# Kernel tuning notes

Measured on AMD Instinct MI355X. Metric: run time of the kernel, lower is better.

## Reference

```python
import jax, jax.numpy as jnp
import numpy as np

NUM_HEADS = 16
NUM_T = 8
L1D = 16  # img_size // patch_size


def _freqs_1d(dim, end, base=10000.0):
    f = 1.0 / (base ** (jnp.arange(0, dim, 2, dtype=jnp.float32) / dim))  # [dim/2]
    ang = jnp.outer(jnp.arange(end, dtype=jnp.float32), f)                # [end, dim/2]
    return jnp.cos(ang), jnp.sin(ang)


def _freqs_2d(dim, h, w, base=10000.0):
    f = 1.0 / (base ** (jnp.arange(0, dim, 4, dtype=jnp.float32)[: dim // 4] / dim))  # [dim/4]
    ax = jnp.outer(jnp.arange(w, dtype=jnp.float32), f)  # [w, dim/4]
    ay = jnp.outer(jnp.arange(h, dtype=jnp.float32), f)  # [h, dim/4]
    # flatten order: position index = y*w + x
    ang_x = jnp.broadcast_to(ax[None, :, :], (h, w, dim // 4)).reshape(h * w, dim // 4)
    ang_y = jnp.broadcast_to(ay[:, None, :], (h, w, dim // 4)).reshape(h * w, dim // 4)
    ang = jnp.concatenate([ang_x, ang_y], axis=-1)  # [h*w, dim/2]
    return jnp.cos(ang), jnp.sin(ang)


def _rope(x, cos, sin):
    # x: [..., P, d]; cos/sin: [P, d/2]; interleaved complex pairs (x0,x1),(x2,x3),...
    xr, xi = x[..., 0::2], x[..., 1::2]
    or_ = xr * cos - xi * sin
    oi = xr * sin + xi * cos
    return jnp.stack([or_, oi], axis=-1).reshape(x.shape)


def setup_inputs() -> dict:
    key = jax.random.key(0)
    ks = jax.random.split(key, 5)
    H = 1024
    return {
        "x": jax.random.normal(ks[0], (2, 2048, H), dtype=jnp.float32),
        "w_qkv": jax.random.normal(ks[1], (3 * H, H), dtype=jnp.float32) * 0.02,
        "b_qkv": jax.random.normal(ks[2], (3 * H,), dtype=jnp.float32) * 0.02,
        "w_out": jax.random.normal(ks[3], (H, H), dtype=jnp.float32) * 0.02,
        "b_out": jax.random.normal(ks[4], (H,), dtype=jnp.float32) * 0.02,
    }


def reference(x, w_qkv, b_qkv, w_out, b_out):
    B, L, H = x.shape
    n, t = NUM_HEADS, NUM_T
    hd = H // n
    Ls = L // t  # spatial tokens per frame (= L1D*L1D)

    # QKV projection; per-head layout [q|k|v] of size 3*hd (matches torch rearrange+chunk)
    qkv = (x @ w_qkv.T + b_qkv).reshape(B, L, n, 3 * hd)
    q, k, v = qkv[..., :hd], qkv[..., hd:2 * hd], qkv[..., 2 * hd:]

    cos_s, sin_s = _freqs_2d(hd, L1D, L1D)  # [Ls, hd/2]
    cos_t, sin_t = _freqs_1d(hd, t)         # [t, hd/2]

    def to_bntl(a):  # (B, L=t*Ls, n, hd) -> (B, n, t, Ls, hd)
        return a.reshape(B, t, Ls, n, hd).transpose(0, 3, 1, 2, 4)

    q = _rope(to_bntl(q), cos_s, sin_s)
    k = _rope(to_bntl(k), cos_s, sin_s)
    # temporal rope: rotate over t axis
    q = _rope(q.transpose(0, 1, 3, 2, 4), cos_t, sin_t).transpose(0, 1, 3, 2, 4)
    k = _rope(k.transpose(0, 1, 3, 2, 4), cos_t, sin_t).transpose(0, 1, 3, 2, 4)
    q = q.reshape(B, n, L, hd)
    k = k.reshape(B, n, L, hd)
    v = v.transpose(0, 2, 1, 3)  # (B, n, L, hd)

    scores = jnp.einsum('bnqd,bnkd->bnqk', q, k) / jnp.sqrt(jnp.asarray(hd, jnp.float32))
    idx = jnp.arange(L)
    neg = jnp.finfo(jnp.float32).min
    causal = jnp.where(idx[None, :] <= idx[:, None], 0.0, neg)  # [L, L]
    attn = jax.nn.softmax((scores + causal).astype(jnp.float32), axis=-1).astype(x.dtype)

    o = jnp.einsum('bnqk,bnkd->bnqd', attn, v).transpose(0, 2, 1, 3).reshape(B, L, H)
    o = o * jax.nn.sigmoid(o)  # swish
    return o @ w_out.T + b_out
```

## Files before the change

kernel.cpp:

```cpp
#include <hip/hip_runtime.h>
#include <math.h>

#define B_SZ 2
#define L_SEQ 2048
#define H_SZ 1024
#define NH 16
#define HD 64
#define QSCALE 0.18033688011112042f

typedef __attribute__((ext_vector_type(8))) short frag_ab;
typedef __attribute__((ext_vector_type(4))) float frag_cd;
typedef __attribute__((ext_vector_type(8))) unsigned short u16x8;
typedef __attribute__((ext_vector_type(4))) unsigned short u16x4;

__device__ __forceinline__ unsigned short f2bf(float f) {
  unsigned int x = __builtin_bit_cast(unsigned int, f);
  x += 0x7fffu + ((x >> 16) & 1u);
  return (unsigned short)(x >> 16);
}
__device__ __forceinline__ float bf2f(unsigned int u) {
  return __builtin_bit_cast(float, u << 16);
}
__device__ __forceinline__ unsigned int cvt_pk_bf16(float lo, float hi) {
  unsigned int r;
  asm("v_cvt_pk_bf16_f32 %0, %1, %2" : "=v"(r) : "v"(lo), "v"(hi));
  return r;
}
__device__ __forceinline__ void gload16(const void* g, void* l) {
  __builtin_amdgcn_global_load_lds((const __attribute__((address_space(1))) void*)g,
                                   (__attribute__((address_space(3))) void*)l, 16, 0, 0);
}

__device__ __forceinline__ void cvt8(const float* __restrict__ in,
                                     unsigned short* __restrict__ out, int i) {
  float4 a = *(const float4*)&in[i];
  float4 b = *(const float4*)&in[i + 4];
  u16x8 o = {f2bf(a.x), f2bf(a.y), f2bf(a.z), f2bf(a.w),
             f2bf(b.x), f2bf(b.y), f2bf(b.z), f2bf(b.w)};
  *(u16x8*)&out[i] = o;
}

__global__ __launch_bounds__(256) void glue_pre_k(
    const float* __restrict__ x, const float* __restrict__ wq, const float* __restrict__ wo,
    unsigned short* __restrict__ xb, unsigned short* __restrict__ wqb,
    unsigned short* __restrict__ wob, float2* __restrict__ ctab) {
  int bx = blockIdx.x, tid = threadIdx.x;
  if (bx < 256) {
    int idx = bx * 256 + tid;
    int l = idx >> 5, j = idx & 31;
    int ti = l >> 8;
    int s = l & 255;
    float ang_s;
    if (j < 16) ang_s = (float)(s & 15) * powf(10000.f, -(float)j / 16.f);
    else        ang_s = (float)(s >> 4) * powf(10000.f, -(float)(j - 16) / 16.f);
    float ang_t = (float)ti * powf(10000.f, -(float)j / 32.f);
    float a = ang_s + ang_t;
    ctab[idx] = make_float2(cosf(a), sinf(a));
  } else if (bx < 2304) {
    cvt8(x, xb, ((bx - 256) * 256 + tid) * 8);
  } else if (bx < 3840) {
    cvt8(wq, wqb, ((bx - 2304) * 256 + tid) * 8);
  } else {
    cvt8(wo, wob, ((bx - 3840) * 256 + tid) * 8);
  }
}

#define G_ISSUE(k0, bi)                                                        \
  _Pragma("unroll") for (int it = 0; it < 2; ++it) {                           \
    int c = tid + it * 256;                                                    \
    int row = c >> 2, e0 = (c & 3) * 8;                                        \
    gload16(A + (size_t)(m0 + row) * K + (k0) + e0, &As[bi][c * 8]);           \
    gload16(W + (size_t)(n0 + row) * K + (k0) + e0, &Ws[bi][c * 8]);           \
  }

__global__ __launch_bounds__(256) void gemm_qkv_fused_k(
    const unsigned short* __restrict__ A, const unsigned short* __restrict__ W,
    const float* __restrict__ bias, const float2* __restrict__ ctab,
    unsigned short* __restrict__ Qb, unsigned short* __restrict__ Kb,
    unsigned short* __restrict__ Vt) {
  const int K = 1024, N = 3072;
  __shared__ unsigned short As[2][128 * 32];
  __shared__ unsigned short Ws[2][128 * 32];
  const frag_cd fzero = {0.f, 0.f, 0.f, 0.f};
  int tid = threadIdx.x;
  int nbx = N >> 7;
  int nwg = gridDim.x;
  int bid = blockIdx.x;
  int qq = nwg >> 3;
  int bidx = (bid & 7) * qq + (bid >> 3);
  int m0 = (bidx / nbx) * 128, n0 = (bidx % nbx) * 128;
  int w = tid >> 6, lane = tid & 63, t = lane & 15, g = lane >> 4;
  int wm = w >> 1, wn = w & 1;
  frag_cd acc[4][4];
#pragma unroll
  for (int mi = 0; mi < 4; ++mi)
#pragma unroll
    for (int ni = 0; ni < 4; ++ni) acc[mi][ni] = fzero;

  G_ISSUE(0, 0);
  __syncthreads();
  int kb = 0;
  for (int k0 = 0; k0 < K; k0 += 32, kb ^= 1) {
    if (k0 + 32 < K) { G_ISSUE(k0 + 32, kb ^ 1); }
    frag_ab af[4], wf[4];
#pragma unroll
    for (int mi = 0; mi < 4; ++mi)
      af[mi] = *(const frag_ab*)&As[kb][(wm * 64 + mi * 16 + t) * 32 + 8 * g];
#pragma unroll
    for (int ni = 0; ni < 4; ++ni)
      wf[ni] = *(const frag_ab*)&Ws[kb][(wn * 64 + ni * 16 + t) * 32 + 8 * g];
    __builtin_amdgcn_s_setprio(1);
#pragma unroll
    for (int mi = 0; mi < 4; ++mi)
#pragma unroll
      for (int ni = 0; ni < 4; ++ni)
        acc[mi][ni] = __builtin_amdgcn_mfma_f32_16x16x32_bf16(af[mi], wf[ni], acc[mi][ni], 0, 0, 0);
    __builtin_amdgcn_s_setprio(0);
    __syncthreads();
  }

#pragma unroll
  for (int ni = 0; ni < 4; ++ni) {
    int cb = n0 + wn * 64 + ni * 16;
    int region = (cb >> 6) % 3;
    int head = cb / 192;
    int d = (cb & 63) + t;
    float bv = bias[cb + t];
    if (region == 2) {
#pragma unroll
      for (int mi = 0; mi < 4; ++mi) {
        int row0 = m0 + wm * 64 + mi * 16 + g * 4;
        int bb = row0 >> 11, l0 = row0 & 2047;
        u16x4 ov;
#pragma unroll
        for (int r = 0; r < 4; ++r) ov[r] = f2bf(acc[mi][ni][r] + bv);
        *(u16x4*)&Vt[((size_t)((bb * NH + head) * HD + d)) * L_SEQ + l0] = ov;
      }
    } else {
      float qs = (region == 0) ? QSCALE : 1.f;
      float sgn = (t & 1) ? qs : -qs;
      unsigned short* dst = (region == 0) ? Qb : Kb;
      int j = d >> 1;
#pragma unroll
      for (int mi = 0; mi < 4; ++mi) {
        int row0 = m0 + wm * 64 + mi * 16 + g * 4;
        int bb = row0 >> 11, l0 = row0 & 2047;
        size_t obase = ((size_t)(bb * NH + head) * L_SEQ + l0) * HD + d;
#pragma unroll
        for (int r = 0; r < 4; ++r) {
          float v = acc[mi][ni][r] + bv;
          float p = __shfl_xor(v, 1);
          float2 cs = ctab[(l0 + r) * 32 + j];
          float o = v * (cs.x * qs) + p * (cs.y * sgn);
          dst[obase + (size_t)r * HD] = f2bf(o);
        }
      }
    }
  }
}

__global__ __launch_bounds__(256) void gemm_mfma_k(
    const unsigned short* __restrict__ A, const unsigned short* __restrict__ W,
    const float* __restrict__ bias, float* __restrict__ C, int M, int N, int K) {
  __shared__ unsigned short As[2][128 * 32];
  __shared__ unsigned short Ws[2][128 * 32];
  const frag_cd fzero = {0.f, 0.f, 0.f, 0.f};
  int tid = threadIdx.x;
  int nbx = N >> 7;
  int nwg = gridDim.x;
  int bid = blockIdx.x;
  int qq = nwg >> 3;
  int bidx = (bid & 7) * qq + (bid >> 3);
  int m0 = (bidx / nbx) * 128, n0 = (bidx % nbx) * 128;
  int w = tid >> 6, lane = tid & 63, t = lane & 15, g = lane >> 4;
  int wm = w >> 1, wn = w & 1;
  frag_cd acc[4][4];
#pragma unroll
  for (int mi = 0; mi < 4; ++mi)
#pragma unroll
    for (int ni = 0; ni < 4; ++ni) acc[mi][ni] = fzero;

  G_ISSUE(0, 0);
  __syncthreads();
  int kb = 0;
  for (int k0 = 0; k0 < K; k0 += 32, kb ^= 1) {
    if (k0 + 32 < K) { G_ISSUE(k0 + 32, kb ^ 1); }
    frag_ab af[4], wf[4];
#pragma unroll
    for (int mi = 0; mi < 4; ++mi)
      af[mi] = *(const frag_ab*)&As[kb][(wm * 64 + mi * 16 + t) * 32 + 8 * g];
#pragma unroll
    for (int ni = 0; ni < 4; ++ni)
      wf[ni] = *(const frag_ab*)&Ws[kb][(wn * 64 + ni * 16 + t) * 32 + 8 * g];
    __builtin_amdgcn_s_setprio(1);
#pragma unroll
    for (int mi = 0; mi < 4; ++mi)
#pragma unroll
      for (int ni = 0; ni < 4; ++ni)
        acc[mi][ni] = __builtin_amdgcn_mfma_f32_16x16x32_bf16(af[mi], wf[ni], acc[mi][ni], 0, 0, 0);
    __builtin_amdgcn_s_setprio(0);
    __syncthreads();
  }
#pragma unroll
  for (int mi = 0; mi < 4; ++mi)
#pragma unroll
    for (int ni = 0; ni < 4; ++ni) {
      int col = n0 + wn * 64 + ni * 16 + t;
      float bv = bias[col];
#pragma unroll
      for (int r = 0; r < 4; ++r)
        C[(size_t)(m0 + wm * 64 + mi * 16 + g * 4 + r) * N + col] = acc[mi][ni][r] + bv;
    }
}

__device__ __forceinline__ void attn_tile(
    const unsigned short* __restrict__ Ksb, const unsigned short* __restrict__ Vsb,
    unsigned short* __restrict__ pw,
    const frag_ab* qf, frag_cd* oacc, float& l_run,
    int qrow, bool diag, int kt, int t, int g) {
  const frag_cd cinit = {-32.f, -32.f, -32.f, -32.f};
  frag_cd st[4];
  __builtin_amdgcn_s_setprio(1);
#pragma unroll
  for (int kb = 0; kb < 4; ++kb) {
    frag_ab k0f = *(const frag_ab*)&Ksb[(((kb * 16 + t) * 64) + 8 * g) ^ ((t & 7) << 3)];
    frag_ab k1f = *(const frag_ab*)&Ksb[(((kb * 16 + t) * 64) + 32 + 8 * g) ^ ((t & 7) << 3)];
    st[kb] = __builtin_amdgcn_mfma_f32_16x16x32_bf16(k0f, qf[0], cinit, 0, 0, 0);
    st[kb] = __builtin_amdgcn_mfma_f32_16x16x32_bf16(k1f, qf[1], st[kb], 0, 0, 0);
  }
  __builtin_amdgcn_s_setprio(0);
  float sv[16];
#pragma unroll
  for (int kb = 0; kb < 4; ++kb)
#pragma unroll
    for (int r = 0; r < 4; ++r) {
      float x = st[kb][r];
      if (diag && (kt * 64 + kb * 16 + g * 4 + r) > qrow) x = -1e30f;
      sv[kb * 4 + r] = x;
    }
  float psum = 0.f;
  unsigned int pk[8];
#pragma unroll
  for (int i = 0; i < 8; ++i) {
    float p0 = __builtin_amdgcn_exp2f(sv[2 * i]);
    float p1 = __builtin_amdgcn_exp2f(sv[2 * i + 1]);
    psum += p0 + p1;
    pk[i] = cvt_pk_bf16(p0, p1);
  }
  psum += __shfl_xor(psum, 16);
  psum += __shfl_xor(psum, 32);
  l_run += psum;

#pragma unroll
  for (int kb = 0; kb < 4; ++kb) {
    uint2 pr = {pk[kb * 2], pk[kb * 2 + 1]};
    *(uint2*)&pw[(t * 64 + kb * 16 + g * 4) ^ ((t & 7) << 3)] = pr;
  }
  frag_ab pf0 = *(const frag_ab*)&pw[(t * 64 + 8 * g) ^ ((t & 7) << 3)];
  frag_ab pf1 = *(const frag_ab*)&pw[(t * 64 + 32 + 8 * g) ^ ((t & 7) << 3)];
  const frag_cd fzero = {0.f, 0.f, 0.f, 0.f};
  (void)fzero;
  __builtin_amdgcn_s_setprio(1);
#pragma unroll
  for (int db = 0; db < 4; ++db) {
    frag_ab v0f = *(const frag_ab*)&Vsb[(((db * 16 + t) * 64) + 8 * g) ^ ((t & 7) << 3)];
    frag_ab v1f = *(const frag_ab*)&Vsb[(((db * 16 + t) * 64) + 32 + 8 * g) ^ ((t & 7) << 3)];
    oacc[db] = __builtin_amdgcn_mfma_f32_16x16x32_bf16(v0f, pf0, oacc[db], 0, 0, 0);
    oacc[db] = __builtin_amdgcn_mfma_f32_16x16x32_bf16(v1f, pf1, oacc[db], 0, 0, 0);
  }
  __builtin_amdgcn_s_setprio(0);
}

__global__ __launch_bounds__(512) void attn_mfma_k(
    const unsigned short* __restrict__ Qg, const unsigned short* __restrict__ Kg,
    const unsigned short* __restrict__ Vt, unsigned short* __restrict__ Og) {
  __shared__ unsigned short Ks[2][64 * 64];
  __shared__ unsigned short Vs[2][64 * 64];
  __shared__ unsigned short Ps[8][16 * 64];
  const frag_cd fzero = {0.f, 0.f, 0.f, 0.f};
  int bx = blockIdx.x;
  int qtA = bx & 15;
  int n = (bx >> 4) & 15;
  int b = bx >> 8;
  int qtB = 31 - qtA;
  int tid = threadIdx.x;
  int w = tid >> 6, lane = tid & 63, t = lane & 15, g = lane >> 4;
  int side = w >> 2;
  int qt = side ? qtA : qtB;
  size_t kvbase = ((size_t)(b * NH + n)) * L_SEQ * HD;
  int qrow = qt * 64 + (w & 3) * 16 + t;

  const unsigned short* qp = Qg + kvbase + (size_t)qrow * HD;
  frag_ab qf[2] = {*(const frag_ab*)(qp + 8 * g), *(const frag_ab*)(qp + 32 + 8 * g)};

  frag_cd oacc[4];
#pragma unroll
  for (int db = 0; db < 4; ++db) oacc[db] = fzero;
  float l_run = 0.f;

  int srow = tid >> 3, se0 = (tid & 7) * 8;
  int sdst = (srow * 64 + se0) ^ ((srow & 7) << 3);
  u16x8 kreg = *(const u16x8*)(Kg + kvbase + (size_t)srow * HD + se0);
  u16x8 vreg = *(const u16x8*)(Vt + kvbase + (size_t)srow * L_SEQ + se0);
  *(u16x8*)&Ks[0][sdst] = kreg;
  *(u16x8*)&Vs[0][sdst] = vreg;

  for (int kt = 0; kt <= qtB; ++kt) {
    int cur = kt & 1;
    __syncthreads();
    if (kt < qtB) {
      kreg = *(const u16x8*)(Kg + kvbase + (size_t)((kt + 1) * 64 + srow) * HD + se0);
      vreg = *(const u16x8*)(Vt + kvbase + (size_t)srow * L_SEQ + (kt + 1) * 64 + se0);
    }
    if (kt <= qt)
      attn_tile(&Ks[cur][0], &Vs[cur][0], &Ps[w][0], qf, oacc, l_run, qrow,
                kt == qt, kt, t, g);
    if (kt < qtB) {
      int nxt = cur ^ 1;
      *(u16x8*)&Ks[nxt][sdst] = kreg;
      *(u16x8*)&Vs[nxt][sdst] = vreg;
    }
  }

  size_t ob0 = (size_t)b * L_SEQ * H_SZ + n * 64;
  float inv = 1.f / l_run;
#pragma unroll
  for (int db = 0; db < 4; ++db) {
    u16x4 ov;
#pragma unroll
    for (int r = 0; r < 4; ++r) {
      float o = oacc[db][r] * inv;
      o = o / (1.f + __expf(-o));
      ov[r] = f2bf(o);
    }
    *(u16x4*)&Og[ob0 + (size_t)qrow * H_SZ + db * 16 + g * 4] = ov;
  }
}

extern "C" void kernel_launch(void* const* d_in, const int* in_sizes, int n_in,
                              void* d_out, int out_size, void* d_ws, size_t ws_size,
                              hipStream_t stream) {
  const float* x = (const float*)d_in[0];
  const float* w_qkv = (const float*)d_in[1];
  const float* b_qkv = (const float*)d_in[2];
  const float* w_out = (const float*)d_in[3];
  const float* b_out = (const float*)d_in[4];
  float* out = (float*)d_out;

  float* ws = (float*)d_ws;
  float2* ctab = (float2*)ws;
  unsigned short* us = (unsigned short*)(ws + 131072);
  unsigned short* Qb = us;
  unsigned short* Kb = Qb + 4194304;
  unsigned short* Vt = Kb + 4194304;
  unsigned short* Og = Vt + 4194304;
  unsigned short* xb = Og + 4194304;
  unsigned short* wqkvb = xb + 4194304;
  unsigned short* woutb = wqkvb + 3145728;

  glue_pre_k<<<4352, 256, 0, stream>>>(x, w_qkv, w_out, xb, wqkvb, woutb, ctab);

  gemm_qkv_fused_k<<<768, 256, 0, stream>>>(xb, wqkvb, b_qkv, ctab, Qb, Kb, Vt);

  attn_mfma_k<<<B_SZ * NH * 16, 512, 0, stream>>>(Qb, Kb, Vt, Og);

  gemm_mfma_k<<<256, 256, 0, stream>>>(Og, woutb, b_out, out, 4096, 1024, 1024);
}
```

Baseline: 113.1 us.

## Software-pipeline attention QK^T one tile ahead with triple-buffered K/V

The attention loop now computes QK^T scores for the next key tile before doing softmax and PV on the current tile, using a three-slot K/V shared buffer and prefetching two tiles ahead. This is meant to overlap MFMA score work with the exp/pack and PV phase and to cut barrier stalls, at the cost of more registers and LDS. Separately, the RoPE cos/sin table is transposed to a j-major layout so the QKV epilogue reads four consecutive positions with two float4 loads instead of four strided float2 loads.

```diff
diff --git a/kernel.cpp b/kernel.cpp
--- a/kernel.cpp
+++ b/kernel.cpp
@@ -47,7 +47,7 @@
   int bx = blockIdx.x, tid = threadIdx.x;
   if (bx < 256) {
     int idx = bx * 256 + tid;
-    int l = idx >> 5, j = idx & 31;
+    int j = idx >> 11, l = idx & 2047;
     int ti = l >> 8;
     int s = l & 255;
     float ang_s;
@@ -146,12 +146,16 @@
         int row0 = m0 + wm * 64 + mi * 16 + g * 4;
         int bb = row0 >> 11, l0 = row0 & 2047;
         size_t obase = ((size_t)(bb * NH + head) * L_SEQ + l0) * HD + d;
+        const float2* cp = ctab + (size_t)j * 2048 + l0;
+        float4 v01 = *(const float4*)cp;
+        float4 v23 = *(const float4*)(cp + 2);
+        float cvec[4] = {v01.x, v01.z, v23.x, v23.z};
+        float svec[4] = {v01.y, v01.w, v23.y, v23.w};
 #pragma unroll
         for (int r = 0; r < 4; ++r) {
           float v = acc[mi][ni][r] + bv;
           float p = __shfl_xor(v, 1);
-          float2 cs = ctab[(l0 + r) * 32 + j];
-          float o = v * (cs.x * qs) + p * (cs.y * sgn);
+          float o = v * (cvec[r] * qs) + p * (svec[r] * sgn);
           dst[obase + (size_t)r * HD] = f2bf(o);
         }
       }
@@ -213,13 +217,10 @@
     }
 }
 
-__device__ __forceinline__ void attn_tile(
-    const unsigned short* __restrict__ Ksb, const unsigned short* __restrict__ Vsb,
-    unsigned short* __restrict__ pw,
-    const frag_ab* qf, frag_cd* oacc, float& l_run,
-    int qrow, bool diag, int kt, int t, int g) {
+__device__ __forceinline__ void qk_compute(
+    const unsigned short* __restrict__ Ksb, const frag_ab* qf, frag_cd* st,
+    int t, int g) {
   const frag_cd cinit = {-32.f, -32.f, -32.f, -32.f};
-  frag_cd st[4];
   __builtin_amdgcn_s_setprio(1);
 #pragma unroll
   for (int kb = 0; kb < 4; ++kb) {
@@ -229,21 +230,24 @@
     st[kb] = __builtin_amdgcn_mfma_f32_16x16x32_bf16(k1f, qf[1], st[kb], 0, 0, 0);
   }
   __builtin_amdgcn_s_setprio(0);
-  float sv[16];
-#pragma unroll
-  for (int kb = 0; kb < 4; ++kb)
-#pragma unroll
-    for (int r = 0; r < 4; ++r) {
-      float x = st[kb][r];
-      if (diag && (kt * 64 + kb * 16 + g * 4 + r) > qrow) x = -1e30f;
-      sv[kb * 4 + r] = x;
-    }
+}
+
+__device__ __forceinline__ void sm_pv(
+    const unsigned short* __restrict__ Vsb, unsigned short* __restrict__ pw,
+    const frag_cd* st, frag_cd* oacc, float& l_run,
+    int qrow, bool diag, int kt, int t, int g) {
   float psum = 0.f;
   unsigned int pk[8];
 #pragma unroll
   for (int i = 0; i < 8; ++i) {
-    float p0 = __builtin_amdgcn_exp2f(sv[2 * i]);
-    float p1 = __builtin_amdgcn_exp2f(sv[2 * i + 1]);
+    int kb = i >> 1, r0 = (2 * i) & 3;
+    float x0 = st[kb][r0], x1 = st[kb][r0 + 1];
+    if (diag) {
+      if ((kt * 64 + kb * 16 + g * 4 + r0) > qrow) x0 = -1e30f;
+      if ((kt * 64 + kb * 16 + g * 4 + r0 + 1) > qrow) x1 = -1e30f;
+    }
+    float p0 = __builtin_amdgcn_exp2f(x0);
+    float p1 = __builtin_amdgcn_exp2f(x1);
     psum += p0 + p1;
     pk[i] = cvt_pk_bf16(p0, p1);
   }
@@ -258,8 +262,6 @@
   }
   frag_ab pf0 = *(const frag_ab*)&pw[(t * 64 + 8 * g) ^ ((t & 7) << 3)];
   frag_ab pf1 = *(const frag_ab*)&pw[(t * 64 + 32 + 8 * g) ^ ((t & 7) << 3)];
-  const frag_cd fzero = {0.f, 0.f, 0.f, 0.f};
-  (void)fzero;
   __builtin_amdgcn_s_setprio(1);
 #pragma unroll
   for (int db = 0; db < 4; ++db) {
@@ -274,8 +276,8 @@
 __global__ __launch_bounds__(512) void attn_mfma_k(
     const unsigned short* __restrict__ Qg, const unsigned short* __restrict__ Kg,
     const unsigned short* __restrict__ Vt, unsigned short* __restrict__ Og) {
-  __shared__ unsigned short Ks[2][64 * 64];
-  __shared__ unsigned short Vs[2][64 * 64];
+  __shared__ unsigned short Ks[3][64 * 64];
+  __shared__ unsigned short Vs[3][64 * 64];
   __shared__ unsigned short Ps[8][16 * 64];
   const frag_cd fzero = {0.f, 0.f, 0.f, 0.f};
   int bx = blockIdx.x;
@@ -289,6 +291,7 @@
   int qt = side ? qtA : qtB;
   size_t kvbase = ((size_t)(b * NH + n)) * L_SEQ * HD;
   int qrow = qt * 64 + (w & 3) * 16 + t;
+  unsigned short* pw = &Ps[w][0];
 
   const unsigned short* qp = Qg + kvbase + (size_t)qrow * HD;
   frag_ab qf[2] = {*(const frag_ab*)(qp + 8 * g), *(const frag_ab*)(qp + 32 + 8 * g)};
@@ -300,26 +303,37 @@
 
   int srow = tid >> 3, se0 = (tid & 7) * 8;
   int sdst = (srow * 64 + se0) ^ ((srow & 7) << 3);
+
   u16x8 kreg = *(const u16x8*)(Kg + kvbase + (size_t)srow * HD + se0);
   u16x8 vreg = *(const u16x8*)(Vt + kvbase + (size_t)srow * L_SEQ + se0);
   *(u16x8*)&Ks[0][sdst] = kreg;
   *(u16x8*)&Vs[0][sdst] = vreg;
-
+  kreg = *(const u16x8*)(Kg + kvbase + (size_t)(64 + srow) * HD + se0);
+  vreg = *(const u16x8*)(Vt + kvbase + (size_t)srow * L_SEQ + 64 + se0);
+  __syncthreads();
+
+  frag_cd st[4], stN[4];
+  qk_compute(&Ks[0][0], qf, st, t, g);
+
+  int cur = 0;
   for (int kt = 0; kt <= qtB; ++kt) {
-    int cur = kt & 1;
-    __syncthreads();
+    int nxt = (cur == 2) ? 0 : cur + 1;
     if (kt < qtB) {
-      kreg = *(const u16x8*)(Kg + kvbase + (size_t)((kt + 1) * 64 + srow) * HD + se0);
-      vreg = *(const u16x8*)(Vt + kvbase + (size_t)srow * L_SEQ + (kt + 1) * 64 + se0);
-    }
-    if (kt <= qt)
-      attn_tile(&Ks[cur][0], &Vs[cur][0], &Ps[w][0], qf, oacc, l_run, qrow,
-                kt == qt, kt, t, g);
-    if (kt < qtB) {
-      int nxt = cur ^ 1;
       *(u16x8*)&Ks[nxt][sdst] = kreg;
       *(u16x8*)&Vs[nxt][sdst] = vreg;
     }
+    __syncthreads();
+    if (kt + 1 < qtB) {
+      kreg = *(const u16x8*)(Kg + kvbase + (size_t)((kt + 2) * 64 + srow) * HD + se0);
+      vreg = *(const u16x8*)(Vt + kvbase + (size_t)srow * L_SEQ + (kt + 2) * 64 + se0);
+    }
+    if (kt < qtB && kt + 1 <= qt)
+      qk_compute(&Ks[nxt][0], qf, stN, t, g);
+    if (kt <= qt)
+      sm_pv(&Vs[cur][0], pw, st, oacc, l_run, qrow, kt == qt, kt, t, g);
+#pragma unroll
+    for (int kb = 0; kb < 4; ++kb) st[kb] = stN[kb];
+    cur = nxt;
   }
 
   size_t ob0 = (size_t)b * L_SEQ * H_SZ + n * 64;
```

Result: no change. 115.2 us (+1.8%).

## Process four query tiles per attention block and transpose RoPE table layout

Applied to the files above, without the earlier changes.

The attention kernel now has each workgroup handle four query tiles (two long, two short, paired across the causal triangle) instead of two. Each wave keeps two sets of accumulators and two Q fragments, and every K/V tile loaded into shared memory is reused by both. The grid is halved, which roughly halves total K/V global traffic at the cost of higher register pressure and fewer workgroups. Separately, the cos/sin table is stored frequency-major so the QKV epilogue can load four consecutive rows with vector loads, and the masking loop is folded into the exp loop.

```diff
diff --git a/kernel.cpp b/kernel.cpp
--- a/kernel.cpp
+++ b/kernel.cpp
@@ -47,7 +47,7 @@
   int bx = blockIdx.x, tid = threadIdx.x;
   if (bx < 256) {
     int idx = bx * 256 + tid;
-    int l = idx >> 5, j = idx & 31;
+    int j = idx >> 11, l = idx & 2047;
     int ti = l >> 8;
     int s = l & 255;
     float ang_s;
@@ -146,12 +146,16 @@
         int row0 = m0 + wm * 64 + mi * 16 + g * 4;
         int bb = row0 >> 11, l0 = row0 & 2047;
         size_t obase = ((size_t)(bb * NH + head) * L_SEQ + l0) * HD + d;
+        const float2* cp = ctab + (size_t)j * 2048 + l0;
+        float4 v01 = *(const float4*)cp;
+        float4 v23 = *(const float4*)(cp + 2);
+        float cvec[4] = {v01.x, v01.z, v23.x, v23.z};
+        float svec[4] = {v01.y, v01.w, v23.y, v23.w};
 #pragma unroll
         for (int r = 0; r < 4; ++r) {
           float v = acc[mi][ni][r] + bv;
           float p = __shfl_xor(v, 1);
-          float2 cs = ctab[(l0 + r) * 32 + j];
-          float o = v * (cs.x * qs) + p * (cs.y * sgn);
+          float o = v * (cvec[r] * qs) + p * (svec[r] * sgn);
           dst[obase + (size_t)r * HD] = f2bf(o);
         }
       }
@@ -229,21 +233,18 @@
     st[kb] = __builtin_amdgcn_mfma_f32_16x16x32_bf16(k1f, qf[1], st[kb], 0, 0, 0);
   }
   __builtin_amdgcn_s_setprio(0);
-  float sv[16];
-#pragma unroll
-  for (int kb = 0; kb < 4; ++kb)
-#pragma unroll
-    for (int r = 0; r < 4; ++r) {
-      float x = st[kb][r];
-      if (diag && (kt * 64 + kb * 16 + g * 4 + r) > qrow) x = -1e30f;
-      sv[kb * 4 + r] = x;
-    }
   float psum = 0.f;
   unsigned int pk[8];
 #pragma unroll
   for (int i = 0; i < 8; ++i) {
-    float p0 = __builtin_amdgcn_exp2f(sv[2 * i]);
-    float p1 = __builtin_amdgcn_exp2f(sv[2 * i + 1]);
+    int kb = i >> 1, r0 = (2 * i) & 3;
+    float x0 = st[kb][r0], x1 = st[kb][r0 + 1];
+    if (diag) {
+      if ((kt * 64 + kb * 16 + g * 4 + r0) > qrow) x0 = -1e30f;
+      if ((kt * 64 + kb * 16 + g * 4 + r0 + 1) > qrow) x1 = -1e30f;
+    }
+    float p0 = __builtin_amdgcn_exp2f(x0);
+    float p1 = __builtin_amdgcn_exp2f(x1);
     psum += p0 + p1;
     pk[i] = cvt_pk_bf16(p0, p1);
   }
@@ -258,8 +259,6 @@
   }
   frag_ab pf0 = *(const frag_ab*)&pw[(t * 64 + 8 * g) ^ ((t & 7) << 3)];
   frag_ab pf1 = *(const frag_ab*)&pw[(t * 64 + 32 + 8 * g) ^ ((t & 7) << 3)];
-  const frag_cd fzero = {0.f, 0.f, 0.f, 0.f};
-  (void)fzero;
   __builtin_amdgcn_s_setprio(1);
 #pragma unroll
   for (int db = 0; db < 4; ++db) {
@@ -276,27 +275,32 @@
     const unsigned short* __restrict__ Vt, unsigned short* __restrict__ Og) {
   __shared__ unsigned short Ks[2][64 * 64];
   __shared__ unsigned short Vs[2][64 * 64];
-  __shared__ unsigned short Ps[8][16 * 64];
+  __shared__ unsigned short Ps[16][16 * 64];
   const frag_cd fzero = {0.f, 0.f, 0.f, 0.f};
   int bx = blockIdx.x;
-  int qtA = bx & 15;
-  int n = (bx >> 4) & 15;
-  int b = bx >> 8;
-  int qtB = 31 - qtA;
+  int pg = bx & 7;
+  int n = (bx >> 3) & 15;
+  int b = bx >> 7;
   int tid = threadIdx.x;
   int w = tid >> 6, lane = tid & 63, t = lane & 15, g = lane >> 4;
-  int side = w >> 2;
-  int qt = side ? qtA : qtB;
+  int half = w >> 2;
+  int wr = (w & 3) * 16;
+  int qtL = 31 - 2 * pg - half;
+  int qtS = 2 * pg + half;
+  int ktmax = 31 - 2 * pg;
   size_t kvbase = ((size_t)(b * NH + n)) * L_SEQ * HD;
-  int qrow = qt * 64 + (w & 3) * 16 + t;
-
-  const unsigned short* qp = Qg + kvbase + (size_t)qrow * HD;
-  frag_ab qf[2] = {*(const frag_ab*)(qp + 8 * g), *(const frag_ab*)(qp + 32 + 8 * g)};
-
-  frag_cd oacc[4];
-#pragma unroll
-  for (int db = 0; db < 4; ++db) oacc[db] = fzero;
-  float l_run = 0.f;
+  int qrowL = qtL * 64 + wr + t;
+  int qrowS = qtS * 64 + wr + t;
+
+  const unsigned short* qpL = Qg + kvbase + (size_t)qrowL * HD;
+  const unsigned short* qpS = Qg + kvbase + (size_t)qrowS * HD;
+  frag_ab qfL[2] = {*(const frag_ab*)(qpL + 8 * g), *(const frag_ab*)(qpL + 32 + 8 * g)};
+  frag_ab qfS[2] = {*(const frag_ab*)(qpS + 8 * g), *(const frag_ab*)(qpS + 32 + 8 * g)};
+
+  frag_cd oaccL[4], oaccS[4];
+#pragma unroll
+  for (int db = 0; db < 4; ++db) { oaccL[db] = fzero; oaccS[db] = fzero; }
+  float lL = 0.f, lS = 0.f;
 
   int srow = tid >> 3, se0 = (tid & 7) * 8;
   int sdst = (srow * 64 + se0) ^ ((srow & 7) << 3);
@@ -305,17 +309,20 @@
   *(u16x8*)&Ks[0][sdst] = kreg;
   *(u16x8*)&Vs[0][sdst] = vreg;
 
-  for (int kt = 0; kt <= qtB; ++kt) {
+  for (int kt = 0; kt <= ktmax; ++kt) {
     int cur = kt & 1;
     __syncthreads();
-    if (kt < qtB) {
+    if (kt < ktmax) {
       kreg = *(const u16x8*)(Kg + kvbase + (size_t)((kt + 1) * 64 + srow) * HD + se0);
       vreg = *(const u16x8*)(Vt + kvbase + (size_t)srow * L_SEQ + (kt + 1) * 64 + se0);
     }
-    if (kt <= qt)
-      attn_tile(&Ks[cur][0], &Vs[cur][0], &Ps[w][0], qf, oacc, l_run, qrow,
-                kt == qt, kt, t, g);
-    if (kt < qtB) {
+    if (kt <= qtS)
+      attn_tile(&Ks[cur][0], &Vs[cur][0], &Ps[w + 8][0], qfS, oaccS, lS, qrowS,
+                kt == qtS, kt, t, g);
+    if (kt <= qtL)
+      attn_tile(&Ks[cur][0], &Vs[cur][0], &Ps[w][0], qfL, oaccL, lL, qrowL,
+                kt == qtL, kt, t, g);
+    if (kt < ktmax) {
       int nxt = cur ^ 1;
       *(u16x8*)&Ks[nxt][sdst] = kreg;
       *(u16x8*)&Vs[nxt][sdst] = vreg;
@@ -323,17 +330,22 @@
   }
 
   size_t ob0 = (size_t)b * L_SEQ * H_SZ + n * 64;
-  float inv = 1.f / l_run;
-#pragma unroll
-  for (int db = 0; db < 4; ++db) {
-    u16x4 ov;
-#pragma unroll
-    for (int r = 0; r < 4; ++r) {
-      float o = oacc[db][r] * inv;
-      o = o / (1.f + __expf(-o));
-      ov[r] = f2bf(o);
-    }
-    *(u16x4*)&Og[ob0 + (size_t)qrow * H_SZ + db * 16 + g * 4] = ov;
+#pragma unroll
+  for (int side = 0; side < 2; ++side) {
+    frag_cd* oacc = side ? oaccS : oaccL;
+    float inv = 1.f / (side ? lS : lL);
+    int qrow = side ? qrowS : qrowL;
+#pragma unroll
+    for (int db = 0; db < 4; ++db) {
+      u16x4 ov;
+#pragma unroll
+      for (int r = 0; r < 4; ++r) {
+        float o = oacc[db][r] * inv;
+        o = o / (1.f + __expf(-o));
+        ov[r] = f2bf(o);
+      }
+      *(u16x4*)&Og[ob0 + (size_t)qrow * H_SZ + db * 16 + g * 4] = ov;
+    }
   }
 }
 
@@ -362,7 +374,7 @@
 
   gemm_qkv_fused_k<<<768, 256, 0, stream>>>(xb, wqkvb, b_qkv, ctab, Qb, Kb, Vt);
 
-  attn_mfma_k<<<B_SZ * NH * 16, 512, 0, stream>>>(Qb, Kb, Vt, Og);
+  attn_mfma_k<<<B_SZ * NH * 8, 512, 0, stream>>>(Qb, Kb, Vt, Og);
 
   gemm_mfma_k<<<256, 256, 0, stream>>>(Og, woutb, b_out, out, 4096, 1024, 1024);
 }
```

Result: no change. 114.1 us (+0.8%).
